# Kernel tuning notes

Hardware: AMD Instinct MI355X
Metric: run time of the kernel (lower is better)

Reference implementation:

```python
import jax, jax.numpy as jnp
import numpy as np
from jax.scipy.special import logsumexp

EPS = 1e-6
SINKHORN_ITERS = 8
TEMPERATURE = 1.0


def sinkhorn(logits):
    # log(clamp(t, min=eps)) / temperature, then alternating row/col log-normalization
    t = jnp.log(jnp.clip(logits, EPS)) / TEMPERATURE
    for _ in range(SINKHORN_ITERS):
        t = t - logsumexp(t, axis=-2, keepdims=True)  # over tokens n
        t = t - logsumexp(t, axis=-1, keepdims=True)  # over experts e
    return jnp.exp(t)


def setup_inputs() -> dict:
    key = jax.random.key(0)
    k1, k2, k3 = jax.random.split(key, 3)
    b, n, d, e, h = 4, 4096, 1024, 8, 1
    x = jax.random.normal(k1, (b, n, d), dtype=jnp.float32)
    gate_w = jax.random.normal(k2, (h, d, e), dtype=jnp.float32)  # to_gate_weight
    experts = jax.random.normal(k3, (e, d, d), dtype=jnp.float32) * 0.02  # expert weight tensor [e, i, o]
    return {"x": x, "gate_w": gate_w, "experts": experts}


def reference(x, gate_w, experts):
    b, n, d = x.shape
    h, _, e = gate_w.shape
    m = n // e  # tokens_per_expert

    xh = x[:, None]  # b 1 n d  (single-headed path)

    # gate logits: b h n e
    gate_logits = jnp.einsum('bhnd,hde->bhne', xh, gate_w)

    # competitive sinkhorn gates (eval mode, no gumbel noise)
    gates = sinkhorn(gate_logits)

    # topk over token dim (dim=-2) with k = tokens_per_expert
    g = jnp.swapaxes(gates, -1, -2)          # b h e n
    gv, idx = jax.lax.top_k(g, m)            # b h e m
    gate_values = jnp.swapaxes(gv, -1, -2)   # b h m e
    routed_indices = jnp.swapaxes(idx, -1, -2)  # b h m e

    # eval + competitive -> hard gates
    hard_gates = (gate_values > 0.5).astype(x.dtype)  # b h m e

    # gather routed tokens: routed[b,h,m,e,d] = x[b,h,idx[b,h,m,e],d]
    bi = jnp.arange(b)[:, None, None, None]
    hi = jnp.arange(h)[None, :, None, None]
    routed = xh[bi, hi, routed_indices]  # b h m e d

    # per-expert GEMM, vectorized over experts: experts [e,i,o] -> [e,h,i,o]
    experts4 = experts[:, None, :, :]
    out = jnp.einsum('bhmei,ehio->bhmeo', routed, experts4)  # b h m e o

    # weight by gates
    out = out * hard_gates[..., None]

    # scatter back (set semantics, as in einx set_at)
    y = jnp.zeros_like(xh).at[bi, hi, routed_indices].set(out)  # b h n d
    return y[:, 0]  # b n d
```

## Files before the change

kernel.cpp:

```cpp
#include <hip/hip_runtime.h>
#include <hip/hip_bf16.h>
#include <stdint.h>

#define BB 4
#define NN 4096
#define DD 1024
#define EE 8
#define MM 512
#define BN (BB*NN)

#define SBLK 32
#define SPB  8
#define SROWS 512

#define FRONT_GATE 512
#define FRONT_CONV 2048
#define FRONT_INIT 64
#define FRONT_BLKS (FRONT_GATE + FRONT_CONV + FRONT_INIT)

typedef __bf16 bf16x8 __attribute__((ext_vector_type(8)));
typedef float  floatx4 __attribute__((ext_vector_type(4)));

typedef const __attribute__((address_space(1))) void* gptr_t;
typedef __attribute__((address_space(3))) void* lptr_t;

__device__ __forceinline__ unsigned short f2bf(float f) {
    union { float f; unsigned u; } v; v.f = f;
    unsigned r = v.u + 0x7fffu + ((v.u >> 16) & 1u);
    return (unsigned short)(r >> 16);
}

__device__ __forceinline__ float gate_reduce8(const float acc[8], int lane) {
    float k1[4];
#pragma unroll
    for (int e = 0; e < 4; e++) {
        float a = acc[e]     + __shfl_xor(acc[e],     1, 64);
        float b = acc[e + 4] + __shfl_xor(acc[e + 4], 1, 64);
        k1[e] = (lane & 1) ? b : a;
    }
    float k2[2];
#pragma unroll
    for (int e = 0; e < 2; e++) {
        float a = k1[e]     + __shfl_xor(k1[e],     2, 64);
        float b = k1[e + 2] + __shfl_xor(k1[e + 2], 2, 64);
        k2[e] = (lane & 2) ? b : a;
    }
    float a = k2[0] + __shfl_xor(k2[0], 4, 64);
    float b = k2[1] + __shfl_xor(k2[1], 4, 64);
    float v = (lane & 4) ? b : a;
    v += __shfl_xor(v, 8, 64);
    v += __shfl_xor(v, 16, 64);
    v += __shfl_xor(v, 32, 64);
    return v;
}

#define OFF_GATES   0u
#define OFF_TOPK    524288u
#define OFF_WIN     589824u
#define OFF_COUNTS  655360u
#define OFF_LISTS   655616u
#define OFF_FLAGS   721152u
#define OFF_PART    737536u
#define OFF_KEYS    753920u
#define OFF_XBF     1802496u
#define OFF_EXPT    35356928u
#define WS_NEEDED   52134144u

__global__ __launch_bounds__(256, 2) void front_kernel(const float* __restrict__ x,
                                                       const float* __restrict__ gw,
                                                       const float* __restrict__ E,
                                                       float* __restrict__ tmat,
                                                       unsigned short* __restrict__ xbf,
                                                       unsigned short* __restrict__ expt,
                                                       int* __restrict__ counts,
                                                       unsigned* __restrict__ flags) {
    __shared__ float tile[64][65];
    int bid = blockIdx.x;
    int tid = threadIdx.x;

    if (bid < FRONT_GATE) {
        int wave = tid >> 6, lane = tid & 63;
        float4 g0[4][4], g1[4][4];
#pragma unroll
        for (int j = 0; j < 4; j++)
#pragma unroll
            for (int r = 0; r < 4; r++) {
                const float4* p = (const float4*)(gw + (size_t)(j * 256 + lane * 4 + r) * 8);
                g0[j][r] = p[0];
                g1[j][r] = p[1];
            }
        int tok0 = (bid * 4 + wave) * 8;
        int exp_id = ((lane & 1) << 2) | (lane & 2) | ((lane & 4) >> 2);
        for (int tt = 0; tt < 8; tt += 2) {
            int tokA = tok0 + tt, tokB = tokA + 1;
            const float4* xrA = (const float4*)(x + (size_t)tokA * DD);
            const float4* xrB = (const float4*)(x + (size_t)tokB * DD);
            float4 xa[4], xc[4];
#pragma unroll
            for (int j = 0; j < 4; j++) xa[j] = xrA[j * 64 + lane];
#pragma unroll
            for (int j = 0; j < 4; j++) xc[j] = xrB[j * 64 + lane];
            if (xbf) {
#pragma unroll
                for (int j = 0; j < 4; j++) {
                    ushort4 o;
                    o.x = f2bf(xa[j].x); o.y = f2bf(xa[j].y); o.z = f2bf(xa[j].z); o.w = f2bf(xa[j].w);
                    ((ushort4*)(xbf + (size_t)tokA * DD))[j * 64 + lane] = o;
                }
#pragma unroll
                for (int j = 0; j < 4; j++) {
                    ushort4 o;
                    o.x = f2bf(xc[j].x); o.y = f2bf(xc[j].y); o.z = f2bf(xc[j].z); o.w = f2bf(xc[j].w);
                    ((ushort4*)(xbf + (size_t)tokB * DD))[j * 64 + lane] = o;
                }
            }
            float accA[8] = {0.f, 0.f, 0.f, 0.f, 0.f, 0.f, 0.f, 0.f};
            float accB[8] = {0.f, 0.f, 0.f, 0.f, 0.f, 0.f, 0.f, 0.f};
#pragma unroll
            for (int j = 0; j < 4; j++) {
                accA[0] += xa[j].x * g0[j][0].x + xa[j].y * g0[j][1].x + xa[j].z * g0[j][2].x + xa[j].w * g0[j][3].x;
                accA[1] += xa[j].x * g0[j][0].y + xa[j].y * g0[j][1].y + xa[j].z * g0[j][2].y + xa[j].w * g0[j][3].y;
                accA[2] += xa[j].x * g0[j][0].z + xa[j].y * g0[j][1].z + xa[j].z * g0[j][2].z + xa[j].w * g0[j][3].z;
                accA[3] += xa[j].x * g0[j][0].w + xa[j].y * g0[j][1].w + xa[j].z * g0[j][2].w + xa[j].w * g0[j][3].w;
                accA[4] += xa[j].x * g1[j][0].x + xa[j].y * g1[j][1].x + xa[j].z * g1[j][2].x + xa[j].w * g1[j][3].x;
                accA[5] += xa[j].x * g1[j][0].y + xa[j].y * g1[j][1].y + xa[j].z * g1[j][2].y + xa[j].w * g1[j][3].y;
                accA[6] += xa[j].x * g1[j][0].z + xa[j].y * g1[j][1].z + xa[j].z * g1[j][2].z + xa[j].w * g1[j][3].z;
                accA[7] += xa[j].x * g1[j][0].w + xa[j].y * g1[j][1].w + xa[j].z * g1[j][2].w + xa[j].w * g1[j][3].w;
                accB[0] += xc[j].x * g0[j][0].x + xc[j].y * g0[j][1].x + xc[j].z * g0[j][2].x + xc[j].w * g0[j][3].x;
                accB[1] += xc[j].x * g0[j][0].y + xc[j].y * g0[j][1].y + xc[j].z * g0[j][2].y + xc[j].w * g0[j][3].y;
                accB[2] += xc[j].x * g0[j][0].z + xc[j].y * g0[j][1].z + xc[j].z * g0[j][2].z + xc[j].w * g0[j][3].z;
                accB[3] += xc[j].x * g0[j][0].w + xc[j].y * g0[j][1].w + xc[j].z * g0[j][2].w + xc[j].w * g0[j][3].w;
                accB[4] += xc[j].x * g1[j][0].x + xc[j].y * g1[j][1].x + xc[j].z * g1[j][2].x + xc[j].w * g1[j][3].x;
                accB[5] += xc[j].x * g1[j][0].y + xc[j].y * g1[j][1].y + xc[j].z * g1[j][2].y + xc[j].w * g1[j][3].y;
                accB[6] += xc[j].x * g1[j][0].z + xc[j].y * g1[j][1].z + xc[j].z * g1[j][2].z + xc[j].w * g1[j][3].z;
                accB[7] += xc[j].x * g1[j][0].w + xc[j].y * g1[j][1].w + xc[j].z * g1[j][2].w + xc[j].w * g1[j][3].w;
            }
            float vA = gate_reduce8(accA, lane);
            float vB = gate_reduce8(accB, lane);
            if (lane < 8) {
                tmat[(size_t)tokA * EE + exp_id] = logf(fmaxf(vA, 1e-6f));
                tmat[(size_t)tokB * EE + exp_id] = logf(fmaxf(vB, 1e-6f));
            }
        }
    } else if (bid < FRONT_GATE + FRONT_CONV) {
        if (!expt) return;
        int cb = bid - FRONT_GATE;
        int e = cb >> 8, t = cb & 255;
        int k0 = (t >> 4) * 64, c0 = (t & 15) * 64;
#pragma unroll
        for (int ii = 0; ii < 4; ii++) {
            int r = (tid >> 4) + ii * 16;
            int c4 = (tid & 15) * 4;
            float4 v = *(const float4*)(E + ((size_t)e * DD + k0 + r) * DD + c0 + c4);
            tile[r][c4 + 0] = v.x; tile[r][c4 + 1] = v.y; tile[r][c4 + 2] = v.z; tile[r][c4 + 3] = v.w;
        }
        __syncthreads();
        int cc = tid >> 2, kk0 = (tid & 3) * 16;
#pragma unroll
        for (int q = 0; q < 4; q++) {
            ushort4 o;
            o.x = f2bf(tile[kk0 + q * 4 + 0][cc]);
            o.y = f2bf(tile[kk0 + q * 4 + 1][cc]);
            o.z = f2bf(tile[kk0 + q * 4 + 2][cc]);
            o.w = f2bf(tile[kk0 + q * 4 + 3][cc]);
            *(ushort4*)&expt[((size_t)e * DD + c0 + cc) * DD + k0 + kk0 + q * 4] = o;
        }
    } else {
        int i = (bid - FRONT_GATE - FRONT_CONV) * 256 + tid;
        if (i < 32) counts[i] = 0;
        if (i < 4096) flags[i] = 0u;
    }
}

__global__ __launch_bounds__(512) void sinkhorn_mb(const float* __restrict__ tmat,
                                                   float* __restrict__ part,
                                                   unsigned* __restrict__ flags,
                                                   unsigned long long* __restrict__ keys,
                                                   int* __restrict__ rank) {
    int g = blockIdx.x;
    int b = g >> 3, sl = g & 7;
    int tid = threadIdx.x;
    int wave = tid >> 6, lane = tid & 63;
    int row = sl * SROWS + tid;
    const float* tr = tmat + ((size_t)b * NN + row) * EE;
    float tv[EE];
#pragma unroll
    for (int e = 0; e < EE; e++) tv[e] = tr[e];

    __shared__ float red[8][8];
    __shared__ float bcm[8];

    for (int it = 0; it < 8; it++) {
#pragma unroll
        for (int e = 0; e < EE; e++) {
            float s = expf(tv[e]);
            for (int off = 32; off > 0; off >>= 1) s += __shfl_down(s, off, 64);
            if (lane == 0) red[wave][e] = s;
        }
        __syncthreads();
        if (tid == 0) {
            float* pm = part + (size_t)(it * 32 + b * 8 + sl) * 16;
#pragma unroll
            for (int e = 0; e < EE; e++) {
                float s = 0.f;
#pragma unroll
                for (int w = 0; w < 8; w++) s += red[w][e];
                __hip_atomic_store(&pm[e], s, __ATOMIC_RELAXED, __HIP_MEMORY_SCOPE_AGENT);
            }
            __hip_atomic_store(&flags[(size_t)(it * 32 + b * 8 + sl) * 16], 1u,
                               __ATOMIC_RELEASE, __HIP_MEMORY_SCOPE_AGENT);
        }
        if (tid < 8) {
            const unsigned* f = flags + (size_t)(it * 32 + b * 8 + tid) * 16;
            while (__hip_atomic_load(f, __ATOMIC_ACQUIRE, __HIP_MEMORY_SCOPE_AGENT) == 0u)
                __builtin_amdgcn_s_sleep(1);
        }
        __syncthreads();
        if (tid < 8) {
            const float* pb = part + (size_t)(it * 32 + b * 8) * 16;
            float s = 0.f;
#pragma unroll
            for (int p = 0; p < SPB; p++)
                s += __hip_atomic_load(&pb[p * 16 + tid], __ATOMIC_RELAXED, __HIP_MEMORY_SCOPE_AGENT);
            bcm[tid] = logf(s);
        }
        __syncthreads();
#pragma unroll
        for (int e = 0; e < EE; e++) tv[e] -= bcm[e];
        {
            float s = 0.f;
#pragma unroll
            for (int e = 0; e < EE; e++) s += expf(tv[e]);
            float lse = logf(s);
#pragma unroll
            for (int e = 0; e < EE; e++) tv[e] -= lse;
        }
    }
#pragma unroll
    for (int e = 0; e < EE; e++) {
        unsigned fb = __float_as_uint(expf(tv[e]));
        keys[(size_t)(b * EE + e) * NN + row] =
            ((unsigned long long)fb << 32) | (unsigned)(~row);
    }
    {
        int4* rz = (int4*)(rank + (size_t)b * EE * NN) + (size_t)sl * (EE * NN / 8 / 4);
        int4 z4 = make_int4(0, 0, 0, 0);
        rz[tid * 2 + 0] = z4;
        rz[tid * 2 + 1] = z4;
    }
}

__global__ __launch_bounds__(256) void rank_count_kernel(const unsigned long long* __restrict__ keys,
                                                         int* __restrict__ rank) {
    int be = blockIdx.y;
    int tid = threadIdx.x;
    int t = blockIdx.x * 256 + tid;
    const unsigned long long* kcol = keys + (size_t)be * NN;
    unsigned long long my = kcol[t];
    const unsigned long long* ks = kcol + (size_t)blockIdx.z * (NN / 4);

    int c0 = 0, c1 = 0, c2 = 0, c3 = 0;
    for (int j = 0; j < NN / 4; j += 16) {
#pragma unroll
        for (int i = 0; i < 16; i += 4) {
            c0 += (int)(ks[j + i + 0] > my);
            c1 += (int)(ks[j + i + 1] > my);
            c2 += (int)(ks[j + i + 2] > my);
            c3 += (int)(ks[j + i + 3] > my);
        }
    }
    atomicAdd(&rank[(size_t)be * NN + t], (c0 + c1) + (c2 + c3));
}

__global__ __launch_bounds__(256) void build_zero_kernel(const unsigned long long* __restrict__ keys,
                                                         const int* __restrict__ rank,
                                                         int* __restrict__ counts,
                                                         int* __restrict__ lists,
                                                         float* __restrict__ y) {
    __shared__ int act_s[64];
    int base = blockIdx.x * 64;
    int tid = threadIdx.x;
    if (tid < 64) {
        int i = base + tid;
        int b = i >> 12, tok = i & 4095;
        int wmax = -1;
#pragma unroll
        for (int e = 0; e < EE; e++) {
            int r = rank[(size_t)(b * 8 + e) * NN + tok];
            if (r < MM) {
                int w = r * 8 + e;
                wmax = wmax > w ? wmax : w;
            }
        }
        int active = 0;
        if (wmax >= 0) {
            int ew = wmax & 7;
            unsigned hi = (unsigned)(keys[(size_t)(b * 8 + ew) * NN + tok] >> 32);
            if (__uint_as_float(hi) > 0.5f) {
                int p = atomicAdd(&counts[b * 8 + ew], 1);
                lists[(b * 8 + ew) * MM + p] = tok;
                active = 1;
            }
        }
        act_s[tid] = active;
    }
    __syncthreads();
    float4 z = make_float4(0.f, 0.f, 0.f, 0.f);
    for (int r = 0; r < 64; r++) {
        if (!act_s[r])
            ((float4*)(y + (size_t)(base + r) * DD))[tid] = z;
    }
}

__global__ __launch_bounds__(256) void expert_gemm_mfma(const unsigned short* __restrict__ xbf,
                                                        const unsigned short* __restrict__ expt,
                                                        const int* __restrict__ counts,
                                                        const int* __restrict__ lists,
                                                        float* __restrict__ y) {
    int be = blockIdx.z;
    int b = be >> 3, e = be & 7;
    int cnt = counts[be];
    int row0 = blockIdx.y * 64;
    if (row0 >= cnt) return;
    int col0 = blockIdx.x * 128;

    __shared__ unsigned short As[64 * 32];
    __shared__ unsigned short Bs[128 * 32];
    __shared__ int toks[64];

    int tid = threadIdx.x;
    int wave = tid >> 6, lane = tid & 63;
    int m16 = lane & 15, quad = lane >> 4;
    int wave_m = wave >> 1, wave_n = wave & 1;

    if (tid < 64) {
        int r = row0 + tid;
        toks[tid] = lists[be * MM + (r < cnt ? r : cnt - 1)];
    }

    int r0 = tid >> 2;
    int ch = tid & 3;

    const unsigned short* xb = xbf + (size_t)b * NN * DD;
    const unsigned short* Eb = expt + (size_t)e * DD * DD;

    floatx4 acc[2][4];
#pragma unroll
    for (int i = 0; i < 2; i++)
#pragma unroll
        for (int j = 0; j < 4; j++) acc[i][j] = (floatx4)0.f;

    for (int k0 = 0; k0 < DD; k0 += 32) {
        __syncthreads();
        {
            const unsigned short* gA  = xb + (size_t)toks[r0] * DD + k0 + ch * 8;
            const unsigned short* gB0 = Eb + (size_t)(col0 + r0) * DD + k0 + ch * 8;
            const unsigned short* gB1 = Eb + (size_t)(col0 + 64 + r0) * DD + k0 + ch * 8;
            __builtin_amdgcn_global_load_lds((gptr_t)gA,  (lptr_t)(As + (size_t)tid * 8), 16, 0, 0);
            __builtin_amdgcn_global_load_lds((gptr_t)gB0, (lptr_t)(Bs + (size_t)tid * 8), 16, 0, 0);
            __builtin_amdgcn_global_load_lds((gptr_t)gB1, (lptr_t)(Bs + 64 * 32 + (size_t)tid * 8), 16, 0, 0);
        }
        __syncthreads();
        bf16x8 af[2], bfr[4];
#pragma unroll
        for (int i = 0; i < 2; i++)
            af[i] = *(const bf16x8*)&As[(wave_m * 32 + i * 16 + m16) * 32 + quad * 8];
#pragma unroll
        for (int j = 0; j < 4; j++)
            bfr[j] = *(const bf16x8*)&Bs[(wave_n * 64 + j * 16 + m16) * 32 + quad * 8];
#pragma unroll
        for (int i = 0; i < 2; i++)
#pragma unroll
            for (int j = 0; j < 4; j++)
                acc[i][j] = __builtin_amdgcn_mfma_f32_16x16x32_bf16(af[i], bfr[j], acc[i][j], 0, 0, 0);
    }

#pragma unroll
    for (int i = 0; i < 2; i++) {
#pragma unroll
        for (int r = 0; r < 4; r++) {
            int lr = wave_m * 32 + i * 16 + quad * 4 + r;
            if (row0 + lr < cnt) {
                int tok = toks[lr];
                float* yr = y + ((size_t)b * NN + tok) * DD + col0 + wave_n * 64 + m16;
#pragma unroll
                for (int j = 0; j < 4; j++) yr[j * 16] = acc[i][j][r];
            }
        }
    }
}

__global__ __launch_bounds__(256) void expert_gemm_kernel(const float* __restrict__ x,
                                                          const float* __restrict__ experts,
                                                          const int* __restrict__ counts,
                                                          const int* __restrict__ lists,
                                                          float* __restrict__ y) {
    int be = blockIdx.z;
    int b = be >> 3, e = be & 7;
    int cnt = counts[be];
    int row0 = blockIdx.y * 64;
    if (row0 >= cnt) return;
    int col0 = blockIdx.x * 64;
    __shared__ float As2[16][68];
    __shared__ float Bs2[16][68];
    __shared__ int toks[64];
    int tid = threadIdx.x;
    if (tid < 64) {
        int r = row0 + tid;
        toks[tid] = (r < cnt) ? lists[be * MM + r] : -1;
    }
    __syncthreads();
    int tx = tid & 15, ty = tid >> 4;
    int ar = tid >> 2;
    int ak = (tid & 3) * 4;
    int bk = tid >> 4;
    int bc4 = (tid & 15) * 4;
    int atok = toks[ar];
    const float* xb = x + (size_t)b * NN * DD;
    const float* Eb = experts + (size_t)e * DD * DD + col0;
    float acc[4][4] = {};
    for (int k0 = 0; k0 < DD; k0 += 16) {
        float4 av;
        if (atok >= 0) av = *(const float4*)(xb + (size_t)atok * DD + k0 + ak);
        else av = make_float4(0.f, 0.f, 0.f, 0.f);
        float4 bv = *(const float4*)(Eb + (size_t)(k0 + bk) * DD + bc4);
        __syncthreads();
        As2[ak + 0][ar] = av.x; As2[ak + 1][ar] = av.y; As2[ak + 2][ar] = av.z; As2[ak + 3][ar] = av.w;
        *(float4*)&Bs2[bk][bc4] = bv;
        __syncthreads();
#pragma unroll
        for (int kk = 0; kk < 16; kk++) {
            float4 a = *(const float4*)&As2[kk][ty * 4];
            float4 bb = *(const float4*)&Bs2[kk][tx * 4];
            acc[0][0] += a.x * bb.x; acc[0][1] += a.x * bb.y; acc[0][2] += a.x * bb.z; acc[0][3] += a.x * bb.w;
            acc[1][0] += a.y * bb.x; acc[1][1] += a.y * bb.y; acc[1][2] += a.y * bb.z; acc[1][3] += a.y * bb.w;
            acc[2][0] += a.z * bb.x; acc[2][1] += a.z * bb.y; acc[2][2] += a.z * bb.z; acc[2][3] += a.z * bb.w;
            acc[3][0] += a.w * bb.x; acc[3][1] += a.w * bb.y; acc[3][2] += a.w * bb.z; acc[3][3] += a.w * bb.w;
        }
    }
#pragma unroll
    for (int i = 0; i < 4; i++) {
        int rl = ty * 4 + i;
        if (row0 + rl < cnt) {
            int tok = toks[rl];
            float4 o = make_float4(acc[i][0], acc[i][1], acc[i][2], acc[i][3]);
            *(float4*)(y + ((size_t)b * NN + tok) * DD + col0 + tx * 4) = o;
        }
    }
}

extern "C" void kernel_launch(void* const* d_in, const int* in_sizes, int n_in,
                              void* d_out, int out_size, void* d_ws, size_t ws_size,
                              hipStream_t stream) {
    const float* x       = (const float*)d_in[0];
    const float* gw      = (const float*)d_in[1];
    const float* experts = (const float*)d_in[2];
    float* y = (float*)d_out;

    char* ws = (char*)d_ws;
    float*    gates    = (float*)(ws + OFF_GATES);
    int*      rank     = (int*)(ws + OFF_GATES);
    int*      counts   = (int*)(ws + OFF_COUNTS);
    int*      lists    = (int*)(ws + OFF_LISTS);
    unsigned* flags    = (unsigned*)(ws + OFF_FLAGS);
    float*    part     = (float*)(ws + OFF_PART);
    unsigned long long* keys = (unsigned long long*)(ws + OFF_KEYS);
    bool big = ws_size >= WS_NEEDED;
    unsigned short* xbf  = big ? (unsigned short*)(ws + OFF_XBF)  : nullptr;
    unsigned short* expt = big ? (unsigned short*)(ws + OFF_EXPT) : nullptr;

    front_kernel<<<FRONT_BLKS, 256, 0, stream>>>(x, gw, experts, gates, xbf, expt,
                                                 counts, flags);
    sinkhorn_mb<<<SBLK, 512, 0, stream>>>(gates, part, flags, keys, rank);
    rank_count_kernel<<<dim3(16, 32, 4), 256, 0, stream>>>(keys, rank);
    build_zero_kernel<<<256, 256, 0, stream>>>(keys, rank, counts, lists, y);
    if (big)
        expert_gemm_mfma<<<dim3(8, 8, BB * EE), 256, 0, stream>>>(xbf, expt, counts, lists, y);
    else
        expert_gemm_kernel<<<dim3(16, 8, BB * EE), 256, 0, stream>>>(x, experts, counts, lists, y);
}
```

Baseline: 282.4 us.

## Overlap expert-weight bf16 conversion with sinkhorn blocks and prefetch gate inputs

The expert-weight transpose-and-convert work moves out of the front kernel into the same launch as the sinkhorn blocks. The bandwidth-heavy conversion can then run on otherwise idle CUs while the 32 latency-bound, flag-synchronised sinkhorn blocks iterate. The gate kernel now software-prefetches the next token pair's x rows, and the counter/flag init collapses into a single extra block. The conversion tiles use 512 threads with 8 elements each. The risk is that the spinning sinkhorn blocks need co-residency, and they now share the launch with 2048 other blocks.

```diff
diff --git a/kernel.cpp b/kernel.cpp
--- a/kernel.cpp
+++ b/kernel.cpp
@@ -15,8 +15,6 @@
 
 #define FRONT_GATE 512
 #define FRONT_CONV 2048
-#define FRONT_INIT 64
-#define FRONT_BLKS (FRONT_GATE + FRONT_CONV + FRONT_INIT)
 
 typedef __bf16 bf16x8 __attribute__((ext_vector_type(8)));
 typedef float  floatx4 __attribute__((ext_vector_type(4)));
@@ -55,8 +53,6 @@
 }
 
 #define OFF_GATES   0u
-#define OFF_TOPK    524288u
-#define OFF_WIN     589824u
 #define OFF_COUNTS  655360u
 #define OFF_LISTS   655616u
 #define OFF_FLAGS   721152u
@@ -66,129 +62,142 @@
 #define OFF_EXPT    35356928u
 #define WS_NEEDED   52134144u
 
-__global__ __launch_bounds__(256, 2) void front_kernel(const float* __restrict__ x,
-                                                       const float* __restrict__ gw,
-                                                       const float* __restrict__ E,
-                                                       float* __restrict__ tmat,
-                                                       unsigned short* __restrict__ xbf,
-                                                       unsigned short* __restrict__ expt,
-                                                       int* __restrict__ counts,
-                                                       unsigned* __restrict__ flags) {
+__global__ __launch_bounds__(256, 2) void gate_kernel(const float* __restrict__ x,
+                                                      const float* __restrict__ gw,
+                                                      float* __restrict__ tmat,
+                                                      unsigned short* __restrict__ xbf,
+                                                      int* __restrict__ counts,
+                                                      unsigned* __restrict__ flags) {
+    int bid = blockIdx.x;
+    int tid = threadIdx.x;
+    if (bid >= FRONT_GATE) {
+        if (tid < 32) counts[tid] = 0;
+        for (int i = tid; i < 4096; i += 256) flags[i] = 0u;
+        return;
+    }
+    int wave = tid >> 6, lane = tid & 63;
+    float4 g0[4][4], g1[4][4];
+#pragma unroll
+    for (int j = 0; j < 4; j++)
+#pragma unroll
+        for (int r = 0; r < 4; r++) {
+            const float4* p = (const float4*)(gw + (size_t)(j * 256 + lane * 4 + r) * 8);
+            g0[j][r] = p[0];
+            g1[j][r] = p[1];
+        }
+    int tok0 = (bid * 4 + wave) * 8;
+    int exp_id = ((lane & 1) << 2) | (lane & 2) | ((lane & 4) >> 2);
+
+    float4 xa[4], xc[4], na[4], nc[4];
+    {
+        const float4* xr = (const float4*)(x + (size_t)tok0 * DD);
+#pragma unroll
+        for (int j = 0; j < 4; j++) xa[j] = xr[j * 64 + lane];
+#pragma unroll
+        for (int j = 0; j < 4; j++) xc[j] = xr[256 + j * 64 + lane];
+    }
+#pragma unroll
+    for (int tt = 0; tt < 8; tt += 2) {
+        int tokA = tok0 + tt, tokB = tokA + 1;
+        if (tt < 6) {
+            const float4* xrn = (const float4*)(x + (size_t)(tokA + 2) * DD);
+#pragma unroll
+            for (int j = 0; j < 4; j++) na[j] = xrn[j * 64 + lane];
+#pragma unroll
+            for (int j = 0; j < 4; j++) nc[j] = xrn[256 + j * 64 + lane];
+        }
+        if (xbf) {
+#pragma unroll
+            for (int j = 0; j < 4; j++) {
+                ushort4 o;
+                o.x = f2bf(xa[j].x); o.y = f2bf(xa[j].y); o.z = f2bf(xa[j].z); o.w = f2bf(xa[j].w);
+                ((ushort4*)(xbf + (size_t)tokA * DD))[j * 64 + lane] = o;
+            }
+#pragma unroll
+            for (int j = 0; j < 4; j++) {
+                ushort4 o;
+                o.x = f2bf(xc[j].x); o.y = f2bf(xc[j].y); o.z = f2bf(xc[j].z); o.w = f2bf(xc[j].w);
+                ((ushort4*)(xbf + (size_t)tokB * DD))[j * 64 + lane] = o;
+            }
+        }
+        float accA[8] = {0.f, 0.f, 0.f, 0.f, 0.f, 0.f, 0.f, 0.f};
+        float accB[8] = {0.f, 0.f, 0.f, 0.f, 0.f, 0.f, 0.f, 0.f};
+#pragma unroll
+        for (int j = 0; j < 4; j++) {
+            accA[0] += xa[j].x * g0[j][0].x + xa[j].y * g0[j][1].x + xa[j].z * g0[j][2].x + xa[j].w * g0[j][3].x;
+            accA[1] += xa[j].x * g0[j][0].y + xa[j].y * g0[j][1].y + xa[j].z * g0[j][2].y + xa[j].w * g0[j][3].y;
+            accA[2] += xa[j].x * g0[j][0].z + xa[j].y * g0[j][1].z + xa[j].z * g0[j][2].z + xa[j].w * g0[j][3].z;
+            accA[3] += xa[j].x * g0[j][0].w + xa[j].y * g0[j][1].w + xa[j].z * g0[j][2].w + xa[j].w * g0[j][3].w;
+            accA[4] += xa[j].x * g1[j][0].x + xa[j].y * g1[j][1].x + xa[j].z * g1[j][2].x + xa[j].w * g1[j][3].x;
+            accA[5] += xa[j].x * g1[j][0].y + xa[j].y * g1[j][1].y + xa[j].z * g1[j][2].y + xa[j].w * g1[j][3].y;
+            accA[6] += xa[j].x * g1[j][0].z + xa[j].y * g1[j][1].z + xa[j].z * g1[j][2].z + xa[j].w * g1[j][3].z;
+            accA[7] += xa[j].x * g1[j][0].w + xa[j].y * g1[j][1].w + xa[j].z * g1[j][2].w + xa[j].w * g1[j][3].w;
+            accB[0] += xc[j].x * g0[j][0].x + xc[j].y * g0[j][1].x + xc[j].z * g0[j][2].x + xc[j].w * g0[j][3].x;
+            accB[1] += xc[j].x * g0[j][0].y + xc[j].y * g0[j][1].y + xc[j].z * g0[j][2].y + xc[j].w * g0[j][3].y;
+            accB[2] += xc[j].x * g0[j][0].z + xc[j].y * g0[j][1].z + xc[j].z * g0[j][2].z + xc[j].w * g0[j][3].z;
+            accB[3] += xc[j].x * g0[j][0].w + xc[j].y * g0[j][1].w + xc[j].z * g0[j][2].w + xc[j].w * g0[j][3].w;
+            accB[4] += xc[j].x * g1[j][0].x + xc[j].y * g1[j][1].x + xc[j].z * g1[j][2].x + xc[j].w * g1[j][3].x;
+            accB[5] += xc[j].x * g1[j][0].y + xc[j].y * g1[j][1].y + xc[j].z * g1[j][2].y + xc[j].w * g1[j][3].y;
+            accB[6] += xc[j].x * g1[j][0].z + xc[j].y * g1[j][1].z + xc[j].z * g1[j][2].z + xc[j].w * g1[j][3].z;
+            accB[7] += xc[j].x * g1[j][0].w + xc[j].y * g1[j][1].w + xc[j].z * g1[j][2].w + xc[j].w * g1[j][3].w;
+        }
+        float vA = gate_reduce8(accA, lane);
+        float vB = gate_reduce8(accB, lane);
+        if (lane < 8) {
+            tmat[(size_t)tokA * EE + exp_id] = logf(fmaxf(vA, 1e-6f));
+            tmat[(size_t)tokB * EE + exp_id] = logf(fmaxf(vB, 1e-6f));
+        }
+        if (tt < 6) {
+#pragma unroll
+            for (int j = 0; j < 4; j++) { xa[j] = na[j]; xc[j] = nc[j]; }
+        }
+    }
+}
+
+__global__ void sinkhorn_conv(const float* __restrict__ tmat,
+                              float* __restrict__ part,
+                              unsigned* __restrict__ flags,
+                              unsigned long long* __restrict__ keys,
+                              int* __restrict__ rank,
+                              const float* __restrict__ E,
+                              unsigned short* __restrict__ expt) {
     __shared__ float tile[64][65];
-    int bid = blockIdx.x;
-    int tid = threadIdx.x;
-
-    if (bid < FRONT_GATE) {
-        int wave = tid >> 6, lane = tid & 63;
-        float4 g0[4][4], g1[4][4];
-#pragma unroll
-        for (int j = 0; j < 4; j++)
-#pragma unroll
-            for (int r = 0; r < 4; r++) {
-                const float4* p = (const float4*)(gw + (size_t)(j * 256 + lane * 4 + r) * 8);
-                g0[j][r] = p[0];
-                g1[j][r] = p[1];
-            }
-        int tok0 = (bid * 4 + wave) * 8;
-        int exp_id = ((lane & 1) << 2) | (lane & 2) | ((lane & 4) >> 2);
-        for (int tt = 0; tt < 8; tt += 2) {
-            int tokA = tok0 + tt, tokB = tokA + 1;
-            const float4* xrA = (const float4*)(x + (size_t)tokA * DD);
-            const float4* xrB = (const float4*)(x + (size_t)tokB * DD);
-            float4 xa[4], xc[4];
-#pragma unroll
-            for (int j = 0; j < 4; j++) xa[j] = xrA[j * 64 + lane];
-#pragma unroll
-            for (int j = 0; j < 4; j++) xc[j] = xrB[j * 64 + lane];
-            if (xbf) {
-#pragma unroll
-                for (int j = 0; j < 4; j++) {
-                    ushort4 o;
-                    o.x = f2bf(xa[j].x); o.y = f2bf(xa[j].y); o.z = f2bf(xa[j].z); o.w = f2bf(xa[j].w);
-                    ((ushort4*)(xbf + (size_t)tokA * DD))[j * 64 + lane] = o;
-                }
-#pragma unroll
-                for (int j = 0; j < 4; j++) {
-                    ushort4 o;
-                    o.x = f2bf(xc[j].x); o.y = f2bf(xc[j].y); o.z = f2bf(xc[j].z); o.w = f2bf(xc[j].w);
-                    ((ushort4*)(xbf + (size_t)tokB * DD))[j * 64 + lane] = o;
-                }
-            }
-            float accA[8] = {0.f, 0.f, 0.f, 0.f, 0.f, 0.f, 0.f, 0.f};
-            float accB[8] = {0.f, 0.f, 0.f, 0.f, 0.f, 0.f, 0.f, 0.f};
-#pragma unroll
-            for (int j = 0; j < 4; j++) {
-                accA[0] += xa[j].x * g0[j][0].x + xa[j].y * g0[j][1].x + xa[j].z * g0[j][2].x + xa[j].w * g0[j][3].x;
-                accA[1] += xa[j].x * g0[j][0].y + xa[j].y * g0[j][1].y + xa[j].z * g0[j][2].y + xa[j].w * g0[j][3].y;
-                accA[2] += xa[j].x * g0[j][0].z + xa[j].y * g0[j][1].z + xa[j].z * g0[j][2].z + xa[j].w * g0[j][3].z;
-                accA[3] += xa[j].x * g0[j][0].w + xa[j].y * g0[j][1].w + xa[j].z * g0[j][2].w + xa[j].w * g0[j][3].w;
-                accA[4] += xa[j].x * g1[j][0].x + xa[j].y * g1[j][1].x + xa[j].z * g1[j][2].x + xa[j].w * g1[j][3].x;
-                accA[5] += xa[j].x * g1[j][0].y + xa[j].y * g1[j][1].y + xa[j].z * g1[j][2].y + xa[j].w * g1[j][3].y;
-                accA[6] += xa[j].x * g1[j][0].z + xa[j].y * g1[j][1].z + xa[j].z * g1[j][2].z + xa[j].w * g1[j][3].z;
-                accA[7] += xa[j].x * g1[j][0].w + xa[j].y * g1[j][1].w + xa[j].z * g1[j][2].w + xa[j].w * g1[j][3].w;
-                accB[0] += xc[j].x * g0[j][0].x + xc[j].y * g0[j][1].x + xc[j].z * g0[j][2].x + xc[j].w * g0[j][3].x;
-                accB[1] += xc[j].x * g0[j][0].y + xc[j].y * g0[j][1].y + xc[j].z * g0[j][2].y + xc[j].w * g0[j][3].y;
-                accB[2] += xc[j].x * g0[j][0].z + xc[j].y * g0[j][1].z + xc[j].z * g0[j][2].z + xc[j].w * g0[j][3].z;
-                accB[3] += xc[j].x * g0[j][0].w + xc[j].y * g0[j][1].w + xc[j].z * g0[j][2].w + xc[j].w * g0[j][3].w;
-                accB[4] += xc[j].x * g1[j][0].x + xc[j].y * g1[j][1].x + xc[j].z * g1[j][2].x + xc[j].w * g1[j][3].x;
-                accB[5] += xc[j].x * g1[j][0].y + xc[j].y * g1[j][1].y + xc[j].z * g1[j][2].y + xc[j].w * g1[j][3].y;
-                accB[6] += xc[j].x * g1[j][0].z + xc[j].y * g1[j][1].z + xc[j].z * g1[j][2].z + xc[j].w * g1[j][3].z;
-                accB[7] += xc[j].x * g1[j][0].w + xc[j].y * g1[j][1].w + xc[j].z * g1[j][2].w + xc[j].w * g1[j][3].w;
-            }
-            float vA = gate_reduce8(accA, lane);
-            float vB = gate_reduce8(accB, lane);
-            if (lane < 8) {
-                tmat[(size_t)tokA * EE + exp_id] = logf(fmaxf(vA, 1e-6f));
-                tmat[(size_t)tokB * EE + exp_id] = logf(fmaxf(vB, 1e-6f));
-            }
-        }
-    } else if (bid < FRONT_GATE + FRONT_CONV) {
+    __shared__ float red[8][8];
+    __shared__ float bcm[8];
+    int g = blockIdx.x;
+    int tid = threadIdx.x;
+
+    if (g >= SBLK) {
         if (!expt) return;
-        int cb = bid - FRONT_GATE;
+        int cb = g - SBLK;
         int e = cb >> 8, t = cb & 255;
         int k0 = (t >> 4) * 64, c0 = (t & 15) * 64;
-#pragma unroll
-        for (int ii = 0; ii < 4; ii++) {
-            int r = (tid >> 4) + ii * 16;
-            int c4 = (tid & 15) * 4;
-            float4 v = *(const float4*)(E + ((size_t)e * DD + k0 + r) * DD + c0 + c4);
-            tile[r][c4 + 0] = v.x; tile[r][c4 + 1] = v.y; tile[r][c4 + 2] = v.z; tile[r][c4 + 3] = v.w;
-        }
-        __syncthreads();
-        int cc = tid >> 2, kk0 = (tid & 3) * 16;
-#pragma unroll
-        for (int q = 0; q < 4; q++) {
-            ushort4 o;
-            o.x = f2bf(tile[kk0 + q * 4 + 0][cc]);
-            o.y = f2bf(tile[kk0 + q * 4 + 1][cc]);
-            o.z = f2bf(tile[kk0 + q * 4 + 2][cc]);
-            o.w = f2bf(tile[kk0 + q * 4 + 3][cc]);
-            *(ushort4*)&expt[((size_t)e * DD + c0 + cc) * DD + k0 + kk0 + q * 4] = o;
-        }
-    } else {
-        int i = (bid - FRONT_GATE - FRONT_CONV) * 256 + tid;
-        if (i < 32) counts[i] = 0;
-        if (i < 4096) flags[i] = 0u;
-    }
-}
-
-__global__ __launch_bounds__(512) void sinkhorn_mb(const float* __restrict__ tmat,
-                                                   float* __restrict__ part,
-                                                   unsigned* __restrict__ flags,
-                                                   unsigned long long* __restrict__ keys,
-                                                   int* __restrict__ rank) {
-    int g = blockIdx.x;
+        int r = tid >> 3, c8 = (tid & 7) * 8;
+        const float* src = E + ((size_t)e * DD + k0 + r) * DD + c0 + c8;
+        float4 v0 = *(const float4*)src;
+        float4 v1 = *(const float4*)(src + 4);
+        tile[r][c8 + 0] = v0.x; tile[r][c8 + 1] = v0.y; tile[r][c8 + 2] = v0.z; tile[r][c8 + 3] = v0.w;
+        tile[r][c8 + 4] = v1.x; tile[r][c8 + 5] = v1.y; tile[r][c8 + 6] = v1.z; tile[r][c8 + 7] = v1.w;
+        __syncthreads();
+        int cc = tid >> 3, kk8 = (tid & 7) * 8;
+        ushort4 o0, o1;
+        o0.x = f2bf(tile[kk8 + 0][cc]); o0.y = f2bf(tile[kk8 + 1][cc]);
+        o0.z = f2bf(tile[kk8 + 2][cc]); o0.w = f2bf(tile[kk8 + 3][cc]);
+        o1.x = f2bf(tile[kk8 + 4][cc]); o1.y = f2bf(tile[kk8 + 5][cc]);
+        o1.z = f2bf(tile[kk8 + 6][cc]); o1.w = f2bf(tile[kk8 + 7][cc]);
+        unsigned short* dst = expt + ((size_t)e * DD + c0 + cc) * DD + k0 + kk8;
+        *(ushort4*)dst = o0;
+        *(ushort4*)(dst + 4) = o1;
+        return;
+    }
+
     int b = g >> 3, sl = g & 7;
-    int tid = threadIdx.x;
     int wave = tid >> 6, lane = tid & 63;
     int row = sl * SROWS + tid;
     const float* tr = tmat + ((size_t)b * NN + row) * EE;
     float tv[EE];
 #pragma unroll
     for (int e = 0; e < EE; e++) tv[e] = tr[e];
-
-    __shared__ float red[8][8];
-    __shared__ float bcm[8];
 
     for (int it = 0; it < 8; it++) {
 #pragma unroll
@@ -469,9 +478,9 @@
     unsigned short* xbf  = big ? (unsigned short*)(ws + OFF_XBF)  : nullptr;
     unsigned short* expt = big ? (unsigned short*)(ws + OFF_EXPT) : nullptr;
 
-    front_kernel<<<FRONT_BLKS, 256, 0, stream>>>(x, gw, experts, gates, xbf, expt,
-                                                 counts, flags);
-    sinkhorn_mb<<<SBLK, 512, 0, stream>>>(gates, part, flags, keys, rank);
+    gate_kernel<<<FRONT_GATE + 1, 256, 0, stream>>>(x, gw, gates, xbf, counts, flags);
+    sinkhorn_conv<<<SBLK + FRONT_CONV, 512, 0, stream>>>(gates, part, flags, keys, rank,
+                                                         experts, expt);
     rank_count_kernel<<<dim3(16, 32, 4), 256, 0, stream>>>(keys, rank);
     build_zero_kernel<<<256, 256, 0, stream>>>(keys, rank, counts, lists, y);
     if (big)
```

Result: no change. 280.5 us (-0.7%).
